# Optimization experiments

Hardware: AMD Instinct MI355X
Metric: run time of the kernel (lower is better)

The kernel has to match this reference:

```python
import jax, jax.numpy as jnp
import numpy as np

ZETA = 1.0  # NeuralStatusRegister zeta (MinArchitecture hardcodes 1.0 for 'nsr')
BATCH, SEQ = 65536, 512


def setup_inputs() -> dict:
    key = jax.random.key(0)
    k0, k1, k2, k3, k4 = jax.random.split(key, 5)
    # xavier_normal for (2,1): std = sqrt(2/(2+1))
    std21 = float(np.sqrt(2.0 / 3.0))
    std11 = 1.0  # (1,1) xavier std = sqrt(2/2) = 1
    return {
        "X": jax.random.normal(k0, (BATCH, SEQ), dtype=jnp.float32),
        "Woperand1": jax.random.normal(k1, (2, 1), dtype=jnp.float32) * std21,
        "Woperand2": jax.random.normal(k2, (2, 1), dtype=jnp.float32) * std21,
        "bias": jnp.zeros((1, 1), dtype=jnp.float32),
        "Wzero": jax.random.normal(k3, (1, 1), dtype=jnp.float32) * std11,
        "Wsign": jax.random.normal(k4, (1, 1), dtype=jnp.float32) * std11,
    }


def reference(X, Woperand1, Woperand2, bias, Wzero, Wsign):
    # operand-selection softmaxes over the storage axis (size 2)
    o1sel = jax.nn.softmax(Woperand1, axis=0)  # (2, 1)
    o2sel = jax.nn.softmax(Woperand2, axis=0)  # (2, 1)
    sel_diff = o1sel - o2sel                    # o1 - o2 = current @ (o1sel - o2sel)

    def step(h, x_t):
        # h: (B, 1) carry; x_t: (B,) current input column
        current = jnp.concatenate([h, x_t[:, None]], axis=1)  # (B, 2)
        x = current @ sel_diff                                 # (B, 1)
        t = jnp.tanh(ZETA * x)
        sign = t @ Wsign                                       # (B, 1)
        zero = (-1.0 + 2.0 * (1.0 - t * t)) @ Wzero            # (B, 1)
        state = jax.nn.sigmoid(bias + sign + zero)             # (B, 1)
        st = jnp.concatenate([state, 1.0 - state], axis=1)     # (B, 2)
        # einsum('bo,bo->b', current, st)[:, None]
        h_new = jnp.sum(current * st, axis=1, keepdims=True)   # (B, 1)
        return h_new, None

    h0 = X[:, 0:1]          # (B, 1)
    xs = X[:, 1:].T         # (SEQ-1, B): scan over time
    h, _ = jax.lax.scan(step, h0, xs)
    return h                # (B, 1)
```

## Files before the change

kernel.cpp:

```cpp
#include <hip/hip_runtime.h>

#define SEQ    512
#define CHUNKS (SEQ / 4)
#define PF     8

__device__ __forceinline__ float stepfn(float h, float xt,
                                        float s0, float c0, float c1, float c2) {
    float d = h - xt;
    float x = s0 * d;
    float e  = __builtin_amdgcn_exp2f(x * 2.8853900817779268f);
    float t  = fmaf(-2.0f, __builtin_amdgcn_rcpf(e + 1.0f), 1.0f);
    float u  = fmaf(t, fmaf(c2, t, c1), c0);
    float e2 = __builtin_amdgcn_exp2f(u * -1.4426950408889634f);
    float g  = __builtin_amdgcn_rcpf(e2 + 1.0f);
    return fmaf(g, d, xt);
}

__global__ __launch_bounds__(256) void scan_kernel(
    const float* __restrict__ X,
    const float* __restrict__ W1,
    const float* __restrict__ W2,
    const float* __restrict__ bias,
    const float* __restrict__ Wzero,
    const float* __restrict__ Wsign,
    float* __restrict__ out, int batch)
{
    int i = blockIdx.x * blockDim.x + threadIdx.x;
    if (i >= batch) return;

    float a1 = 1.0f / (1.0f + __expf(W1[1] - W1[0]));
    float a2 = 1.0f / (1.0f + __expf(W2[1] - W2[0]));
    float s0 = a1 - a2;
    float wz = Wzero[0];
    float c0 = bias[0] + wz;
    float c1 = Wsign[0];
    float c2 = -2.0f * wz;

    const float4* row = (const float4*)(X + (size_t)i * SEQ);

    float4 buf[PF];
    #pragma unroll
    for (int k = 0; k < PF; ++k) buf[k] = row[k];

    float h = 0.0f;
    for (int base = 0; base < CHUNKS; base += PF) {
        #pragma unroll
        for (int k = 0; k < PF; ++k) {
            float4 v = buf[k];
            int n = base + PF + k;
            if (n < CHUNKS) buf[k] = row[n];
            if (k == 0 && base == 0) h = v.x;
            else h = stepfn(h, v.x, s0, c0, c1, c2);
            h = stepfn(h, v.y, s0, c0, c1, c2);
            h = stepfn(h, v.z, s0, c0, c1, c2);
            h = stepfn(h, v.w, s0, c0, c1, c2);
        }
    }
    out[i] = h;
}

extern "C" void kernel_launch(void* const* d_in, const int* in_sizes, int n_in,
                              void* d_out, int out_size, void* d_ws, size_t ws_size,
                              hipStream_t stream) {
    const float* X    = (const float*)d_in[0];
    const float* W1   = (const float*)d_in[1];
    const float* W2   = (const float*)d_in[2];
    const float* bias = (const float*)d_in[3];
    const float* Wz   = (const float*)d_in[4];
    const float* Wsg  = (const float*)d_in[5];
    float* out = (float*)d_out;

    int batch = in_sizes[0] / SEQ;
    dim3 block(256);
    dim3 grid((batch + block.x - 1) / block.x);
    scan_kernel<<<grid, block, 0, stream>>>(X, W1, W2, bias, Wz, Wsg, out, batch);
}
```

Measured before the change: 201.5 us.

## Stage row tiles through LDS for coalesced loads and simplify step math

Before, each thread read its own 2KB row with float4 loads, so the loads within a wavefront were strided and poorly coalesced. Now each wavefront loads a 64-row by 16-column tile cooperatively, 4 lanes per row, and transposes it through padded, double-buffered LDS with register prefetch two tiles ahead. The step function is also rewritten so the tanh/sigmoid chain works directly on the reciprocal with prefolded constants, removing a few FMAs per step. This adds LDS traffic and a layout that assumes the batch is a multiple of 64 rows, with no barrier needed since each wave uses its own buffer.

Result: slower. 217.9 us (+8.2%).

```diff
diff --git a/kernel.cpp b/kernel.cpp
--- a/kernel.cpp
+++ b/kernel.cpp
@@ -1,17 +1,18 @@
 #include <hip/hip_runtime.h>
 
-#define SEQ    512
-#define CHUNKS (SEQ / 4)
-#define PF     8
+#define SEQ     512
+#define TW      16
+#define NT      (SEQ / TW)
+#define STRIDE  20
+#define WBUF    (64 * STRIDE)
 
 __device__ __forceinline__ float stepfn(float h, float xt,
-                                        float s0, float c0, float c1, float c2) {
-    float d = h - xt;
-    float x = s0 * d;
-    float e  = __builtin_amdgcn_exp2f(x * 2.8853900817779268f);
-    float t  = fmaf(-2.0f, __builtin_amdgcn_rcpf(e + 1.0f), 1.0f);
-    float u  = fmaf(t, fmaf(c2, t, c1), c0);
-    float e2 = __builtin_amdgcn_exp2f(u * -1.4426950408889634f);
+                                        float K, float A0, float A1, float A2) {
+    float d  = h - xt;
+    float e  = __builtin_amdgcn_exp2f(K * d);
+    float r  = __builtin_amdgcn_rcpf(e + 1.0f);
+    float w  = fmaf(fmaf(A2, r, A1), r, A0);
+    float e2 = __builtin_amdgcn_exp2f(w);
     float g  = __builtin_amdgcn_rcpf(e2 + 1.0f);
     return fmaf(g, d, xt);
 }
@@ -25,9 +26,14 @@
     const float* __restrict__ Wsign,
     float* __restrict__ out, int batch)
 {
-    int i = blockIdx.x * blockDim.x + threadIdx.x;
-    if (i >= batch) return;
+    __shared__ float lds[2 * 4 * WBUF];
 
+    const int lane = threadIdx.x & 63;
+    const int wid  = threadIdx.x >> 6;
+    const int rowbase = blockIdx.x * 256 + wid * 64;
+    if (rowbase >= batch) return;
+
+    const float L2E = 1.4426950408889634f;
     float a1 = 1.0f / (1.0f + __expf(W1[1] - W1[0]));
     float a2 = 1.0f / (1.0f + __expf(W2[1] - W2[0]));
     float s0 = a1 - a2;
@@ -35,28 +41,76 @@
     float c0 = bias[0] + wz;
     float c1 = Wsign[0];
     float c2 = -2.0f * wz;
+    float K  = 2.0f * s0 * L2E;
+    float A0 = -L2E * (c0 + c1 + c2);
+    float A1 =  L2E * (2.0f * c1 + 4.0f * c2);
+    float A2 = -L2E * (4.0f * c2);
 
-    const float4* row = (const float4*)(X + (size_t)i * SEQ);
+    const int a  = lane >> 2;
+    const int b4 = lane & 3;
+    const float* gp = X + (size_t)(rowbase + a) * SEQ + b4 * 4;
 
-    float4 buf[PF];
+    float4 stg[4];
     #pragma unroll
-    for (int k = 0; k < PF; ++k) buf[k] = row[k];
+    for (int k = 0; k < 4; ++k)
+        stg[k] = *(const float4*)(gp + (size_t)k * 16 * SEQ);
+    {
+        float* w0 = lds + wid * WBUF;
+        #pragma unroll
+        for (int k = 0; k < 4; ++k)
+            *(float4*)(w0 + (a + 16 * k) * STRIDE + b4 * 4) = stg[k];
+    }
+    #pragma unroll
+    for (int k = 0; k < 4; ++k)
+        stg[k] = *(const float4*)(gp + (size_t)k * 16 * SEQ + TW);
 
     float h = 0.0f;
-    for (int base = 0; base < CHUNKS; base += PF) {
-        #pragma unroll
-        for (int k = 0; k < PF; ++k) {
-            float4 v = buf[k];
-            int n = base + PF + k;
-            if (n < CHUNKS) buf[k] = row[n];
-            if (k == 0 && base == 0) h = v.x;
-            else h = stepfn(h, v.x, s0, c0, c1, c2);
-            h = stepfn(h, v.y, s0, c0, c1, c2);
-            h = stepfn(h, v.z, s0, c0, c1, c2);
-            h = stepfn(h, v.w, s0, c0, c1, c2);
+    int bsel = 0;
+    for (int t = 0; t < NT; ++t) {
+        if (t < NT - 1) {
+            float* wb = lds + ((bsel ^ 1) * 4 + wid) * WBUF;
+            #pragma unroll
+            for (int k = 0; k < 4; ++k)
+                *(float4*)(wb + (a + 16 * k) * STRIDE + b4 * 4) = stg[k];
         }
+        if (t < NT - 2) {
+            #pragma unroll
+            for (int k = 0; k < 4; ++k)
+                stg[k] = *(const float4*)(gp + (size_t)k * 16 * SEQ + (size_t)(t + 2) * TW);
+        }
+        const float* rb = lds + (bsel * 4 + wid) * WBUF + lane * STRIDE;
+        float4 q0 = *(const float4*)(rb + 0);
+        float4 q1 = *(const float4*)(rb + 4);
+        float4 q2 = *(const float4*)(rb + 8);
+        float4 q3 = *(const float4*)(rb + 12);
+
+        if (t == 0) {
+            h = q0.x;
+            h = stepfn(h, q0.y, K, A0, A1, A2);
+            h = stepfn(h, q0.z, K, A0, A1, A2);
+            h = stepfn(h, q0.w, K, A0, A1, A2);
+        } else {
+            h = stepfn(h, q0.x, K, A0, A1, A2);
+            h = stepfn(h, q0.y, K, A0, A1, A2);
+            h = stepfn(h, q0.z, K, A0, A1, A2);
+            h = stepfn(h, q0.w, K, A0, A1, A2);
+        }
+        h = stepfn(h, q1.x, K, A0, A1, A2);
+        h = stepfn(h, q1.y, K, A0, A1, A2);
+        h = stepfn(h, q1.z, K, A0, A1, A2);
+        h = stepfn(h, q1.w, K, A0, A1, A2);
+        h = stepfn(h, q2.x, K, A0, A1, A2);
+        h = stepfn(h, q2.y, K, A0, A1, A2);
+        h = stepfn(h, q2.z, K, A0, A1, A2);
+        h = stepfn(h, q2.w, K, A0, A1, A2);
+        h = stepfn(h, q3.x, K, A0, A1, A2);
+        h = stepfn(h, q3.y, K, A0, A1, A2);
+        h = stepfn(h, q3.z, K, A0, A1, A2);
+        h = stepfn(h, q3.w, K, A0, A1, A2);
+
+        bsel ^= 1;
     }
-    out[i] = h;
+    out[rowbase + lane] = h;
 }
 
 extern "C" void kernel_launch(void* const* d_in, const int* in_sizes, int n_in,
@@ -72,6 +126,6 @@
 
     int batch = in_sizes[0] / SEQ;
     dim3 block(256);
-    dim3 grid((batch + block.x - 1) / block.x);
+    dim3 grid((batch + 255) / 256);
     scan_kernel<<<grid, block, 0, stream>>>(X, W1, W2, bias, Wz, Wsg, out, batch);
 }
```
